# Performance work log

Measured on AMD Instinct MI355X. Metric: run time of the kernel, lower is better.

## Reference

```python
import jax, jax.numpy as jnp
import numpy as np

LAM = 0.5
LAG = 1
ALPHA = 0.5
EPS = 1e-8


def setup_inputs() -> dict:
    key = jax.random.key(0)
    k1, k2, k3, k4 = jax.random.split(key, 4)
    B, T, F, H = 64, 4096, 64, 256
    return {
        "input": jax.random.normal(k1, (B, T, 1), dtype=jnp.float32),
        "target": jax.random.normal(k2, (B, T, 1), dtype=jnp.float32),
        "sequence": jax.random.normal(k3, (B, T, F), dtype=jnp.float32),
        "forget_gates": jax.random.uniform(k4, (B, T, H), dtype=jnp.float32),
    }


def reference(input, target, sequence, forget_gates):
    B, T, F = sequence.shape
    x = jnp.moveaxis(sequence, 1, 0)          # [T, B, F] time-major
    x_t = x[LAG:]                              # [T-LAG, B, F]
    x_lag = x[:-LAG]                           # [T-LAG, B, F]

    m0 = jnp.zeros((B, F), dtype=sequence.dtype)
    v0 = jnp.full((B, F), EPS, dtype=sequence.dtype)
    c0 = jnp.zeros((B, F), dtype=sequence.dtype)

    def step(carry, inp):
        m, v, c = carry
        xt, xl = inp
        m = LAM * m + (1.0 - LAM) * xt
        v = LAM * v + (1.0 - LAM) * (xt - m) ** 2
        c = LAM * c + (1.0 - LAM) * (xt - m) * (xl - m)
        ac = c / jnp.sqrt(v * v + EPS)         # matches torch: sqrt(var*var + eps)
        return (m, v, c), ac

    _, acs = jax.lax.scan(step, (m0, v0, c0), (x_t, x_lag))  # [T-LAG, B, F]
    pad = jnp.zeros((LAG, B, F), dtype=sequence.dtype)       # initial_padding zeros
    ac_full = jnp.concatenate([pad, acs], axis=0)            # [T, B, F]

    irrelevance = 1.0 - jnp.abs(ac_full)                     # [T, B, F]
    irrelevance = jnp.mean(irrelevance, axis=2, keepdims=True)  # [T, B, 1]
    irrelevance = jnp.moveaxis(irrelevance, 0, 1)            # [B, T, 1]

    penalty = jnp.mean(irrelevance * forget_gates)
    mse = jnp.mean((input - target) ** 2)
    return mse + ALPHA * penalty
```

## Files before the change

kernel.cpp:

```cpp
#include <hip/hip_runtime.h>

constexpr int B = 64;
constexpr int T = 4096;
constexpr int F = 64;
constexpr int H = 256;
constexpr float EPSC = 1e-8f;
constexpr float ALPHAC = 0.5f;

constexpr int C = 128;
constexpr int W = 48;
constexpr int CHUNKS = T / C;
constexpr int NTASK = B * CHUNKS;
constexpr int K_BLOCKS = NTASK / 4;

#define WS_PEN 0
#define WS_MSE NTASK

__global__ __launch_bounds__(256) void k_fused(
    const float* __restrict__ seq,
    const float* __restrict__ fg,
    const float* __restrict__ inp,
    const float* __restrict__ tgt,
    float* __restrict__ ws) {
  const int lane = threadIdx.x & 63;
  const int task = blockIdx.x * (blockDim.x >> 6) + (threadIdx.x >> 6);
  const int b = task / CHUNKS;
  const int ci = task % CHUNKS;
  const int t0 = ci * C;
  const int tend = t0 + C;

  const float* sp = seq + (size_t)b * T * F + lane;
  const float* gp = fg + (size_t)b * T * H + lane * 4;

  float m = 0.f, v = 0.f, c = 0.f, acc = 0.f;
  float xl = 0.f;

  if (ci == 0) {
    v = EPSC;
  } else {
    const int ts = t0 - W;
    xl = sp[(ts - 1) * F];
    float xw[4];
#pragma unroll
    for (int j = 0; j < 4; ++j) xw[j] = sp[(ts + j) * F];
#pragma unroll
    for (int i = 0; i < W; ++i) {
      const float xt = xw[i & 3];
      if (i + 4 < W) xw[i & 3] = sp[(ts + i + 4) * F];
      m = 0.5f * (m + xt);
      const float d = xt - m;
      v = 0.5f * fmaf(d, d, v);
      c = 0.5f * fmaf(d, xl - m, c);
      xl = xt;
    }
  }

  const int tstart = t0;
  float4 qb[4];
  float xb[4];
#pragma unroll
  for (int j = 0; j < 4; ++j) {
    qb[j] = *reinterpret_cast<const float4*>(gp + (size_t)(tstart + j) * H);
    xb[j] = sp[(tstart + j) * F];
  }

#pragma unroll 4
  for (int i = 0; i < C; ++i) {
    const int tt = tstart + i;
    const float4 q = qb[i & 3];
    const float xt = xb[i & 3];
    int tp = tt + 4;
    tp = (tp < tend) ? tp : (tend - 1);
    qb[i & 3] = *reinterpret_cast<const float4*>(gp + (size_t)tp * H);
    xb[i & 3] = sp[tp * F];

    float s = (q.x + q.y) + (q.z + q.w);
#pragma unroll
    for (int off = 32; off; off >>= 1) s += __shfl_xor(s, off, 64);

    if (tt != 0) {
      m = 0.5f * (m + xt);
      const float d = xt - m;
      v = 0.5f * fmaf(d, d, v);
      c = 0.5f * fmaf(d, xl - m, c);
      const float ac = c * rsqrtf(fmaf(v, v, EPSC));
      acc = fmaf(1.0f - fabsf(ac), s, acc);
    } else {
      acc += s;
    }
    xl = xt;
  }

#pragma unroll
  for (int off = 32; off; off >>= 1) acc += __shfl_xor(acc, off, 64);
  if (lane == 0) ws[WS_PEN + task] = acc;

  float macc = 0.f;
  const int gid = blockIdx.x * blockDim.x + threadIdx.x;
  const int nt = gridDim.x * blockDim.x;
  const int R = B * T;
  for (int i = gid; i < R; i += nt) {
    const float d = inp[i] - tgt[i];
    macc = fmaf(d, d, macc);
  }
#pragma unroll
  for (int off = 32; off; off >>= 1) macc += __shfl_xor(macc, off, 64);
  __shared__ float sm[4];
  if ((threadIdx.x & 63) == 0) sm[threadIdx.x >> 6] = macc;
  __syncthreads();
  if (threadIdx.x == 0)
    ws[WS_MSE + blockIdx.x] = (sm[0] + sm[1]) + (sm[2] + sm[3]);
}

__global__ __launch_bounds__(256) void k_reduce(
    const float* __restrict__ ws,
    float* __restrict__ out) {
  float p = 0.f, mt = 0.f;
#pragma unroll
  for (int i = 0; i < NTASK / 256; ++i)
    p += ws[WS_PEN + threadIdx.x + i * 256];
#pragma unroll
  for (int i = 0; i < K_BLOCKS / 256; ++i)
    mt += ws[WS_MSE + threadIdx.x + i * 256];
#pragma unroll
  for (int off = 32; off; off >>= 1) {
    p += __shfl_xor(p, off, 64);
    mt += __shfl_xor(mt, off, 64);
  }
  __shared__ float sm[8];
  if ((threadIdx.x & 63) == 0) {
    sm[(threadIdx.x >> 6) * 2] = p;
    sm[(threadIdx.x >> 6) * 2 + 1] = mt;
  }
  __syncthreads();
  if (threadIdx.x == 0) {
    const float pt = sm[0] + sm[2] + sm[4] + sm[6];
    const float ms = sm[1] + sm[3] + sm[5] + sm[7];
    const float R = (float)B * (float)T;
    const float pscale = ALPHAC / (R * (float)H * (float)F);
    out[0] = ms / R + pt * pscale;
  }
}

extern "C" void kernel_launch(void* const* d_in, const int* in_sizes, int n_in,
                              void* d_out, int out_size, void* d_ws, size_t ws_size,
                              hipStream_t stream) {
  const float* inp = (const float*)d_in[0];
  const float* tgt = (const float*)d_in[1];
  const float* seq = (const float*)d_in[2];
  const float* fg  = (const float*)d_in[3];
  float* out = (float*)d_out;
  float* ws  = (float*)d_ws;

  k_fused<<<K_BLOCKS, 256, 0, stream>>>(seq, fg, inp, tgt, ws);
  k_reduce<<<1, 256, 0, stream>>>(ws, out);
}
```

Baseline: 407.3 us.

## Split scan and forget-gate dot product into separate kernels

Divides the fused kernel in two. The first kernel runs the sequential scan, reduces the per-timestep irrelevance across features through shared memory, and writes a [B,T] array to the workspace. The second kernel streams the large forget-gate tensor in a flat grid-stride loop and takes its dot product with that array. The goal is to take the 256 MB forget-gate read off the latency-bound scan loop so it can run at full bandwidth. The cost is an extra launch, a small intermediate round trip through memory, and two __syncthreads per tile inside the scan.

```diff
diff --git a/kernel.cpp b/kernel.cpp
--- a/kernel.cpp
+++ b/kernel.cpp
@@ -11,28 +11,31 @@
 constexpr int W = 48;
 constexpr int CHUNKS = T / C;
 constexpr int NTASK = B * CHUNKS;
-constexpr int K_BLOCKS = NTASK / 4;
+constexpr int SCAN_BLOCKS = NTASK / 4;
+constexpr int TILE = 32;
 
-#define WS_PEN 0
-#define WS_MSE NTASK
+constexpr int DOT_BLOCKS = 2048;
 
-__global__ __launch_bounds__(256) void k_fused(
+#define WS_IRR 0
+#define WS_PEN (B * T)
+#define WS_MSE (B * T + DOT_BLOCKS)
+
+__global__ __launch_bounds__(256) void k_scan(
     const float* __restrict__ seq,
-    const float* __restrict__ fg,
     const float* __restrict__ inp,
     const float* __restrict__ tgt,
     float* __restrict__ ws) {
+  __shared__ float lt[4][TILE][65];
   const int lane = threadIdx.x & 63;
-  const int task = blockIdx.x * (blockDim.x >> 6) + (threadIdx.x >> 6);
+  const int wv = threadIdx.x >> 6;
+  const int task = blockIdx.x * 4 + wv;
   const int b = task / CHUNKS;
   const int ci = task % CHUNKS;
   const int t0 = ci * C;
-  const int tend = t0 + C;
 
   const float* sp = seq + (size_t)b * T * F + lane;
-  const float* gp = fg + (size_t)b * T * H + lane * 4;
 
-  float m = 0.f, v = 0.f, c = 0.f, acc = 0.f;
+  float m = 0.f, v = 0.f, c = 0.f;
   float xl = 0.f;
 
   if (ci == 0) {
@@ -55,45 +58,45 @@
     }
   }
 
-  const int tstart = t0;
-  float4 qb[4];
-  float xb[4];
+  float xb[8];
 #pragma unroll
-  for (int j = 0; j < 4; ++j) {
-    qb[j] = *reinterpret_cast<const float4*>(gp + (size_t)(tstart + j) * H);
-    xb[j] = sp[(tstart + j) * F];
+  for (int j = 0; j < 8; ++j) xb[j] = sp[(t0 + j) * F];
+
+  const int tr = lane & 31;
+  const int half = lane >> 5;
+
+  for (int tile = 0; tile < C / TILE; ++tile) {
+    const int ibase = tile * TILE;
+#pragma unroll
+    for (int j = 0; j < TILE; ++j) {
+      const int i = ibase + j;
+      const int tt = t0 + i;
+      const float xt = xb[j & 7];
+      int tp = i + 8;
+      tp = (tp < C) ? tp : (C - 1);
+      xb[j & 7] = sp[(t0 + tp) * F];
+      float w;
+      if (tt != 0) {
+        m = 0.5f * (m + xt);
+        const float d = xt - m;
+        v = 0.5f * fmaf(d, d, v);
+        c = 0.5f * fmaf(d, xl - m, c);
+        const float ac = c * rsqrtf(fmaf(v, v, EPSC));
+        w = 1.0f - fabsf(ac);
+      } else {
+        w = 1.0f;
+      }
+      xl = xt;
+      lt[wv][j][lane] = w;
+    }
+    __syncthreads();
+    float s = 0.f;
+#pragma unroll
+    for (int k = 0; k < 32; ++k) s += lt[wv][tr][half * 32 + k];
+    s += __shfl_xor(s, 32, 64);
+    if (half == 0) ws[WS_IRR + b * T + t0 + ibase + tr] = s;
+    __syncthreads();
   }
-
-#pragma unroll 4
-  for (int i = 0; i < C; ++i) {
-    const int tt = tstart + i;
-    const float4 q = qb[i & 3];
-    const float xt = xb[i & 3];
-    int tp = tt + 4;
-    tp = (tp < tend) ? tp : (tend - 1);
-    qb[i & 3] = *reinterpret_cast<const float4*>(gp + (size_t)tp * H);
-    xb[i & 3] = sp[tp * F];
-
-    float s = (q.x + q.y) + (q.z + q.w);
-#pragma unroll
-    for (int off = 32; off; off >>= 1) s += __shfl_xor(s, off, 64);
-
-    if (tt != 0) {
-      m = 0.5f * (m + xt);
-      const float d = xt - m;
-      v = 0.5f * fmaf(d, d, v);
-      c = 0.5f * fmaf(d, xl - m, c);
-      const float ac = c * rsqrtf(fmaf(v, v, EPSC));
-      acc = fmaf(1.0f - fabsf(ac), s, acc);
-    } else {
-      acc += s;
-    }
-    xl = xt;
-  }
-
-#pragma unroll
-  for (int off = 32; off; off >>= 1) acc += __shfl_xor(acc, off, 64);
-  if (lane == 0) ws[WS_PEN + task] = acc;
 
   float macc = 0.f;
   const int gid = blockIdx.x * blockDim.x + threadIdx.x;
@@ -106,10 +109,34 @@
 #pragma unroll
   for (int off = 32; off; off >>= 1) macc += __shfl_xor(macc, off, 64);
   __shared__ float sm[4];
-  if ((threadIdx.x & 63) == 0) sm[threadIdx.x >> 6] = macc;
+  if (lane == 0) sm[wv] = macc;
   __syncthreads();
   if (threadIdx.x == 0)
     ws[WS_MSE + blockIdx.x] = (sm[0] + sm[1]) + (sm[2] + sm[3]);
+}
+
+__global__ __launch_bounds__(256) void k_dot(
+    const float* __restrict__ fg,
+    float* __restrict__ ws) {
+  const float* __restrict__ irr = ws + WS_IRR;
+  const float4* __restrict__ fg4 = reinterpret_cast<const float4*>(fg);
+  constexpr int N4 = B * T * (H / 4);
+  constexpr int STRIDE = DOT_BLOCKS * 256;
+  const int gid = blockIdx.x * 256 + threadIdx.x;
+  float acc = 0.f;
+#pragma unroll 4
+  for (int i = gid; i < N4; i += STRIDE) {
+    const float4 q = fg4[i];
+    const float r = irr[i >> 6];
+    acc = fmaf((q.x + q.y) + (q.z + q.w), r, acc);
+  }
+#pragma unroll
+  for (int off = 32; off; off >>= 1) acc += __shfl_xor(acc, off, 64);
+  __shared__ float sm[4];
+  if ((threadIdx.x & 63) == 0) sm[threadIdx.x >> 6] = acc;
+  __syncthreads();
+  if (threadIdx.x == 0)
+    ws[WS_PEN + blockIdx.x] = (sm[0] + sm[1]) + (sm[2] + sm[3]);
 }
 
 __global__ __launch_bounds__(256) void k_reduce(
@@ -117,10 +144,10 @@
     float* __restrict__ out) {
   float p = 0.f, mt = 0.f;
 #pragma unroll
-  for (int i = 0; i < NTASK / 256; ++i)
+  for (int i = 0; i < DOT_BLOCKS / 256; ++i)
     p += ws[WS_PEN + threadIdx.x + i * 256];
 #pragma unroll
-  for (int i = 0; i < K_BLOCKS / 256; ++i)
+  for (int i = 0; i < SCAN_BLOCKS / 256; ++i)
     mt += ws[WS_MSE + threadIdx.x + i * 256];
 #pragma unroll
   for (int off = 32; off; off >>= 1) {
@@ -152,6 +179,7 @@
   float* out = (float*)d_out;
   float* ws  = (float*)d_ws;
 
-  k_fused<<<K_BLOCKS, 256, 0, stream>>>(seq, fg, inp, tgt, ws);
+  k_scan<<<SCAN_BLOCKS, 256, 0, stream>>>(seq, inp, tgt, ws);
+  k_dot<<<DOT_BLOCKS, 256, 0, stream>>>(fg, ws);
   k_reduce<<<1, 256, 0, stream>>>(ws, out);
 }
```

Measured after the change: 412.1 us. No clear change (+1.2%).
